# Kernel optimization log

Measured on AMD Instinct MI355X. Metric: run time of the kernel, lower is better.

Reference implementation:

```python
import jax, jax.numpy as jnp
import numpy as np

P = 15          # processor layers
D = 128         # node/edge feature dim (== hidden dim)
N_NODES = 10000
N_EDGES = 160000


def _mlp(x, w0, b0, w1, b1, w2, b2):
    h = jax.nn.relu(x @ w0 + b0)
    h = jax.nn.relu(h @ w1 + b1)
    return h @ w2 + b2


def setup_inputs() -> dict:
    key = jax.random.key(0)
    ks = jax.random.split(key, 20)
    inp = {
        "node_features": jax.random.normal(ks[0], (N_NODES, D), jnp.float32),
        "edge_features": jax.random.normal(ks[1], (N_EDGES, D), jnp.float32),
        "src": jax.random.randint(ks[2], (N_EDGES,), 0, N_NODES, jnp.int32),
        "dst": jax.random.randint(ks[3], (N_EDGES,), 0, N_NODES, jnp.int32),
    }
    s = 0.05
    # edge MLP: input 2*D + D = 384 -> 128 -> 128 -> 128, stacked over P layers
    inp["ew0"] = jax.random.normal(ks[4], (P, 3 * D, D), jnp.float32) * s
    inp["eb0"] = jnp.zeros((P, D), jnp.float32)
    inp["ew1"] = jax.random.normal(ks[5], (P, D, D), jnp.float32) * s
    inp["eb1"] = jnp.zeros((P, D), jnp.float32)
    inp["ew2"] = jax.random.normal(ks[6], (P, D, D), jnp.float32) * s
    inp["eb2"] = jnp.zeros((P, D), jnp.float32)
    # node MLP: input D + D = 256 -> 128 -> 128 -> 128
    inp["nw0"] = jax.random.normal(ks[7], (P, 2 * D, D), jnp.float32) * s
    inp["nb0"] = jnp.zeros((P, D), jnp.float32)
    inp["nw1"] = jax.random.normal(ks[8], (P, D, D), jnp.float32) * s
    inp["nb1"] = jnp.zeros((P, D), jnp.float32)
    inp["nw2"] = jax.random.normal(ks[9], (P, D, D), jnp.float32) * s
    inp["nb2"] = jnp.zeros((P, D), jnp.float32)
    return inp


def reference(node_features, edge_features, src, dst,
              ew0, eb0, ew1, eb1, ew2, eb2,
              nw0, nb0, nw1, nb1, nw2, nb2):
    n, e = node_features, edge_features
    for i in range(P):
        # --- edge block: gather src/dst node feats, edge MLP, residual ---
        cat_e = jnp.concatenate([n[src], n[dst], e], axis=-1)  # [E, 3D]
        e = _mlp(cat_e, ew0[i], eb0[i], ew1[i], eb1[i], ew2[i], eb2[i]) + e
        # --- node block: scatter-sum edges to dst nodes, node MLP, residual ---
        agg = jax.ops.segment_sum(e, dst, num_segments=N_NODES)  # [N, D]
        cat_n = jnp.concatenate([n, agg], axis=-1)               # [N, 2D]
        n = _mlp(cat_n, nw0[i], nb0[i], nw1[i], nb1[i], nw2[i], nb2[i]) + n
    return n
```

## Files before the change

### kernel.cpp

```cpp
#include <hip/hip_runtime.h>

#define DD 128
#define PP 15
#define NNODES 10000
#define NEDGES 160000

typedef __attribute__((ext_vector_type(8))) short bf16x8;
typedef __attribute__((ext_vector_type(4))) float f32x4;

__device__ inline ushort f2bf(float f) {
  unsigned u = __builtin_bit_cast(unsigned, f);
  u += 0x7FFFu + ((u >> 16) & 1u);
  return (ushort)(u >> 16);
}

__device__ inline float bf2f(ushort h) {
  unsigned u = ((unsigned)h) << 16;
  return __builtin_bit_cast(float, u);
}

__device__ inline uint cvt_pk(float lo, float hi) {
  uint r;
  asm("v_cvt_pk_bf16_f32 %0, %1, %2" : "=v"(r) : "v"(lo), "v"(hi));
  return r;
}

__device__ inline f32x4 mfma16(bf16x8 a, bf16x8 b, f32x4 c) {
  return __builtin_amdgcn_mfma_f32_16x16x32_bf16(a, b, c, 0, 0, 0);
}

__global__ __launch_bounds__(256) void pack_all(
    const float* __restrict__ ew0, const float* __restrict__ ew1,
    const float* __restrict__ ew2, const float* __restrict__ nw0,
    const float* __restrict__ nw1, const float* __restrict__ nw2,
    ushort* __restrict__ out) {
  int i = blockIdx.x * 256 + threadIdx.x;
  if (i >= 2211840) return;
  const float* w; int K; int j = i;
  if (i < 737280)       { w = ew0; K = 384; }
  else if (i < 983040)  { w = ew1; K = 128; j = i - 737280; }
  else if (i < 1228800) { w = ew2; K = 128; j = i - 983040; }
  else if (i < 1720320) { w = nw0; K = 256; j = i - 1228800; }
  else if (i < 1966080) { w = nw1; K = 128; j = i - 1720320; }
  else                  { w = nw2; K = 128; j = i - 1966080; }
  int per = K * 128;
  int p = j / per, q = j % per;
  int e = q & 7;
  int lane = (q >> 3) & 63;
  int t = q >> 9;
  int nkt = K >> 5;
  int kt = t % nkt, cb = t / nkt;
  int k = kt * 32 + ((lane >> 4) << 3) + e;
  int n = (cb << 4) + (lane & 15);
  out[i] = f2bf(w[(size_t)p * per + (size_t)k * 128 + n]);
}

__global__ __launch_bounds__(256) void cvt_all(const float* __restrict__ ef,
                                               const float* __restrict__ nf,
                                               ushort* __restrict__ ebf,
                                               float* __restrict__ nbuf,
                                               ushort* __restrict__ nbf) {
  const int en4 = NEDGES * DD / 4;
  const int nn4 = NNODES * DD / 4;
  int i = blockIdx.x * 256 + threadIdx.x;
  if (i < en4) {
    float4 v = ((const float4*)ef)[i];
    ushort4 h;
    h.x = f2bf(v.x); h.y = f2bf(v.y); h.z = f2bf(v.z); h.w = f2bf(v.w);
    ((ushort4*)ebf)[i] = h;
  } else if (i < en4 + nn4) {
    int k = i - en4;
    float4 v = ((const float4*)nf)[k];
    ((float4*)nbuf)[k] = v;
    ushort4 h;
    h.x = f2bf(v.x); h.y = f2bf(v.y); h.z = f2bf(v.z); h.w = f2bf(v.w);
    ((ushort4*)nbf)[k] = h;
  }
}

__global__ __launch_bounds__(256) void hist_kernel(const int* __restrict__ dst,
                                                   int* __restrict__ cnt) {
  int i = blockIdx.x * 256 + threadIdx.x;
  if (i < NEDGES) atomicAdd(&cnt[dst[i]], 1);
}

__global__ __launch_bounds__(256) void scan_kernel(const int* __restrict__ cnt,
                                                   int* __restrict__ row_start,
                                                   int* __restrict__ cursor) {
  __shared__ int part[256];
  const int CH = (NNODES + 255) / 256;
  int t = threadIdx.x;
  int beg = t * CH, end = min(beg + CH, NNODES);
  int s = 0;
  for (int i = beg; i < end; ++i) s += cnt[i];
  part[t] = s;
  __syncthreads();
  for (int off = 1; off < 256; off <<= 1) {
    int v = (t >= off) ? part[t - off] : 0;
    __syncthreads();
    part[t] += v;
    __syncthreads();
  }
  int run = part[t] - s;
  for (int i = beg; i < end; ++i) {
    row_start[i] = run;
    cursor[i] = run;
    run += cnt[i];
  }
  if (t == 255) row_start[NNODES] = NEDGES;
}

__global__ __launch_bounds__(256) void scatter_kernel(const int* __restrict__ dst,
                                                      int* __restrict__ cursor,
                                                      int* __restrict__ eidx) {
  int i = blockIdx.x * 256 + threadIdx.x;
  if (i < NEDGES) {
    int pos = atomicAdd(&cursor[dst[i]], 1);
    eidx[pos] = i;
  }
}

__global__ __launch_bounds__(256) void agg_kernel(const ushort* __restrict__ ebf,
                                                  ushort* __restrict__ abf,
                                                  const int* __restrict__ row_start,
                                                  const int* __restrict__ eidx) {
  int wv = threadIdx.x >> 6, lane = threadIdx.x & 63;
  int node = blockIdx.x * 4 + wv;
  if (node >= NNODES) return;
  int jb = row_start[node], je = row_start[node + 1];
  float ax = 0.f, ay = 0.f, bx = 0.f, by = 0.f;
  float cx = 0.f, cy = 0.f, dx = 0.f, dy = 0.f;
  int j = jb;
  for (; j + 3 < je; j += 4) {
    int e0 = eidx[j], e1 = eidx[j + 1], e2 = eidx[j + 2], e3 = eidx[j + 3];
    uint u0 = *(const uint*)(ebf + (size_t)e0 * DD + lane * 2);
    uint u1 = *(const uint*)(ebf + (size_t)e1 * DD + lane * 2);
    uint u2 = *(const uint*)(ebf + (size_t)e2 * DD + lane * 2);
    uint u3 = *(const uint*)(ebf + (size_t)e3 * DD + lane * 2);
    ax += bf2f((ushort)u0); ay += __builtin_bit_cast(float, u0 & 0xFFFF0000u);
    bx += bf2f((ushort)u1); by += __builtin_bit_cast(float, u1 & 0xFFFF0000u);
    cx += bf2f((ushort)u2); cy += __builtin_bit_cast(float, u2 & 0xFFFF0000u);
    dx += bf2f((ushort)u3); dy += __builtin_bit_cast(float, u3 & 0xFFFF0000u);
  }
  for (; j < je; ++j) {
    int e0 = eidx[j];
    uint u0 = *(const uint*)(ebf + (size_t)e0 * DD + lane * 2);
    ax += bf2f((ushort)u0); ay += __builtin_bit_cast(float, u0 & 0xFFFF0000u);
  }
  float sx = (ax + bx) + (cx + dx);
  float sy = (ay + by) + (cy + dy);
  *(uint*)&abf[(size_t)node * DD + lane * 2] = cvt_pk(sx, sy);
}

__global__ __launch_bounds__(512, 6) void edge_kernel(
    const ushort* __restrict__ nbf, ushort* __restrict__ ebf,
    const int* __restrict__ srcI, const int* __restrict__ dstI,
    const ushort* __restrict__ w0, const float* __restrict__ b0,
    const ushort* __restrict__ w1, const float* __restrict__ b1,
    const ushort* __restrict__ w2, const float* __restrict__ b2) {
  __shared__ ushort S[64 * 384];
  const int tid = threadIdx.x;
  const int e0 = blockIdx.x * 64;
  const int lane = tid & 63, wv = tid >> 6;
  const int l15 = lane & 15, l4 = lane >> 4;

#pragma unroll
  for (int i = 0; i < 6; ++i) {
    int c = i * 512 + tid;
    int row = c / 48, f8 = c % 48;
    const ushort* sp;
    if (f8 < 16)       sp = nbf + (size_t)srcI[e0 + row] * DD + f8 * 8;
    else if (f8 < 32)  sp = nbf + (size_t)dstI[e0 + row] * DD + (f8 - 16) * 8;
    else               sp = ebf + (size_t)(e0 + row) * DD + (f8 - 32) * 8;
    bf16x8 v = *(const bf16x8*)sp;
    *(bf16x8*)&S[row * 384 + ((f8 ^ (row & 15)) * 8)] = v;
  }
  __syncthreads();

  const f32x4 z = {0.f, 0.f, 0.f, 0.f};
  const int cb = wv;
  const int col = cb * 16 + l15;
  f32x4 acc[4];

#pragma unroll
  for (int rb = 0; rb < 4; ++rb) acc[rb] = z;
#pragma unroll
  for (int kt = 0; kt < 12; ++kt) {
    bf16x8 bW = *(const bf16x8*)(w0 + (size_t)((cb * 12 + kt) * 64 + lane) * 8);
#pragma unroll
    for (int rb = 0; rb < 4; ++rb) {
      int row = rb * 16 + l15;
      bf16x8 a = *(const bf16x8*)&S[row * 384 + (((kt * 4 + l4) ^ (row & 15)) * 8)];
      acc[rb] = mfma16(a, bW, acc[rb]);
    }
  }
  __syncthreads();

  {
    float bias = b0[col];
    int cs = col >> 3, c7 = col & 7;
#pragma unroll
    for (int rb = 0; rb < 4; ++rb) {
      float v0 = fmaxf(acc[rb][0] + bias, 0.f);
      float v1 = fmaxf(acc[rb][1] + bias, 0.f);
      float v2 = fmaxf(acc[rb][2] + bias, 0.f);
      float v3 = fmaxf(acc[rb][3] + bias, 0.f);
      uint p01 = cvt_pk(v0, v1), p23 = cvt_pk(v2, v3);
      int r0 = rb * 16 + l4 * 4;
      S[(r0 + 0) * 384 + ((cs ^ ((r0 + 0) & 15)) * 8) + c7] = (ushort)p01;
      S[(r0 + 1) * 384 + ((cs ^ ((r0 + 1) & 15)) * 8) + c7] = (ushort)(p01 >> 16);
      S[(r0 + 2) * 384 + ((cs ^ ((r0 + 2) & 15)) * 8) + c7] = (ushort)p23;
      S[(r0 + 3) * 384 + ((cs ^ ((r0 + 3) & 15)) * 8) + c7] = (ushort)(p23 >> 16);
    }
  }
  __syncthreads();

#pragma unroll
  for (int rb = 0; rb < 4; ++rb) acc[rb] = z;
#pragma unroll
  for (int kt = 0; kt < 4; ++kt) {
    bf16x8 bW = *(const bf16x8*)(w1 + (size_t)((cb * 4 + kt) * 64 + lane) * 8);
#pragma unroll
    for (int rb = 0; rb < 4; ++rb) {
      int row = rb * 16 + l15;
      bf16x8 a = *(const bf16x8*)&S[row * 384 + (((kt * 4 + l4) ^ (row & 15)) * 8)];
      acc[rb] = mfma16(a, bW, acc[rb]);
    }
  }
  {
    float bias = b1[col];
    int cs = col >> 3, c7 = col & 7;
#pragma unroll
    for (int rb = 0; rb < 4; ++rb) {
      float v0 = fmaxf(acc[rb][0] + bias, 0.f);
      float v1 = fmaxf(acc[rb][1] + bias, 0.f);
      float v2 = fmaxf(acc[rb][2] + bias, 0.f);
      float v3 = fmaxf(acc[rb][3] + bias, 0.f);
      uint p01 = cvt_pk(v0, v1), p23 = cvt_pk(v2, v3);
      int r0 = rb * 16 + l4 * 4;
      S[(r0 + 0) * 384 + ((16 + (cs ^ ((r0 + 0) & 15))) * 8) + c7] = (ushort)p01;
      S[(r0 + 1) * 384 + ((16 + (cs ^ ((r0 + 1) & 15))) * 8) + c7] = (ushort)(p01 >> 16);
      S[(r0 + 2) * 384 + ((16 + (cs ^ ((r0 + 2) & 15))) * 8) + c7] = (ushort)p23;
      S[(r0 + 3) * 384 + ((16 + (cs ^ ((r0 + 3) & 15))) * 8) + c7] = (ushort)(p23 >> 16);
    }
  }
  __syncthreads();

#pragma unroll
  for (int rb = 0; rb < 4; ++rb) acc[rb] = z;
#pragma unroll
  for (int kt = 0; kt < 4; ++kt) {
    bf16x8 bW = *(const bf16x8*)(w2 + (size_t)((cb * 4 + kt) * 64 + lane) * 8);
#pragma unroll
    for (int rb = 0; rb < 4; ++rb) {
      int row = rb * 16 + l15;
      bf16x8 a = *(const bf16x8*)&S[row * 384 + ((16 + ((kt * 4 + l4) ^ (row & 15))) * 8)];
      acc[rb] = mfma16(a, bW, acc[rb]);
    }
  }
  {
    float bias = b2[col];
    int cs = col >> 3, c7 = col & 7;
#pragma unroll
    for (int rb = 0; rb < 4; ++rb) {
      int r0 = rb * 16 + l4 * 4;
      int i0 = (r0 + 0) * 384 + ((32 + (cs ^ ((r0 + 0) & 15))) * 8) + c7;
      int i1 = (r0 + 1) * 384 + ((32 + (cs ^ ((r0 + 1) & 15))) * 8) + c7;
      int i2 = (r0 + 2) * 384 + ((32 + (cs ^ ((r0 + 2) & 15))) * 8) + c7;
      int i3 = (r0 + 3) * 384 + ((32 + (cs ^ ((r0 + 3) & 15))) * 8) + c7;
      float v0 = bf2f(S[i0]) + acc[rb][0] + bias;
      float v1 = bf2f(S[i1]) + acc[rb][1] + bias;
      float v2 = bf2f(S[i2]) + acc[rb][2] + bias;
      float v3 = bf2f(S[i3]) + acc[rb][3] + bias;
      uint p01 = cvt_pk(v0, v1), p23 = cvt_pk(v2, v3);
      S[i0] = (ushort)p01;
      S[i1] = (ushort)(p01 >> 16);
      S[i2] = (ushort)p23;
      S[i3] = (ushort)(p23 >> 16);
    }
  }
  __syncthreads();
#pragma unroll
  for (int i = 0; i < 2; ++i) {
    int c = i * 512 + tid;
    int row = c >> 4, f8 = c & 15;
    bf16x8 v = *(const bf16x8*)&S[row * 384 + ((32 + (f8 ^ (row & 15))) * 8)];
    *(bf16x8*)&ebf[(size_t)(e0 + row) * DD + f8 * 8] = v;
  }
}

__global__ __launch_bounds__(256) void node_kernel(
    float* __restrict__ nbuf, ushort* __restrict__ nbf,
    const ushort* __restrict__ abf,
    const ushort* __restrict__ w0, const float* __restrict__ b0,
    const ushort* __restrict__ w1, const float* __restrict__ b1,
    const ushort* __restrict__ w2, const float* __restrict__ b2) {
  __shared__ ushort Alds[32 * 256];
  __shared__ ushort Hlds[32 * 128];
  const int tid = threadIdx.x;
  const int n0 = blockIdx.x * 32;
  const int lane = tid & 63, wv = tid >> 6;
  const int l15 = lane & 15, l4 = lane >> 4;

#pragma unroll
  for (int i = 0; i < 4; ++i) {
    int c = i * 256 + tid;
    int row = c >> 5, f8 = c & 31;
    int node = n0 + row;
    bf16x8 v = {0, 0, 0, 0, 0, 0, 0, 0};
    if (node < NNODES) {
      const ushort* sp = (f8 < 16) ? nbf + (size_t)node * DD + f8 * 8
                                   : abf + (size_t)node * DD + (f8 - 16) * 8;
      v = *(const bf16x8*)sp;
    }
    *(bf16x8*)&Alds[row * 256 + ((f8 ^ (row & 15)) * 8)] = v;
  }
  __syncthreads();

  const f32x4 z = {0.f, 0.f, 0.f, 0.f};
  const int cbA = wv * 2, cbB = wv * 2 + 1;
  f32x4 acc[2][2];

  acc[0][0] = z; acc[0][1] = z; acc[1][0] = z; acc[1][1] = z;
#pragma unroll
  for (int kt = 0; kt < 8; ++kt) {
    bf16x8 bA = *(const bf16x8*)(w0 + (size_t)((cbA * 8 + kt) * 64 + lane) * 8);
    bf16x8 bB = *(const bf16x8*)(w0 + (size_t)((cbB * 8 + kt) * 64 + lane) * 8);
    int sl = ((kt * 4 + l4) ^ l15) * 8;
    bf16x8 a0 = *(const bf16x8*)&Alds[l15 * 256 + sl];
    bf16x8 a1 = *(const bf16x8*)&Alds[(16 + l15) * 256 + sl];
    acc[0][0] = mfma16(a0, bA, acc[0][0]); acc[0][1] = mfma16(a0, bB, acc[0][1]);
    acc[1][0] = mfma16(a1, bA, acc[1][0]); acc[1][1] = mfma16(a1, bB, acc[1][1]);
  }
  {
    float biasA = b0[cbA * 16 + l15], biasB = b0[cbB * 16 + l15];
#pragma unroll
    for (int cbi = 0; cbi < 2; ++cbi) {
      int col = (wv * 2 + cbi) * 16 + l15;
      float bias = cbi ? biasB : biasA;
      int cs = col >> 3, c7 = col & 7;
#pragma unroll
      for (int rb = 0; rb < 2; ++rb) {
        float v0 = fmaxf(acc[rb][cbi][0] + bias, 0.f);
        float v1 = fmaxf(acc[rb][cbi][1] + bias, 0.f);
        float v2 = fmaxf(acc[rb][cbi][2] + bias, 0.f);
        float v3 = fmaxf(acc[rb][cbi][3] + bias, 0.f);
        uint p01 = cvt_pk(v0, v1), p23 = cvt_pk(v2, v3);
        int r0 = rb * 16 + l4 * 4;
        Hlds[(r0 + 0) * 128 + ((cs ^ ((r0 + 0) & 15)) * 8) + c7] = (ushort)p01;
        Hlds[(r0 + 1) * 128 + ((cs ^ ((r0 + 1) & 15)) * 8) + c7] = (ushort)(p01 >> 16);
        Hlds[(r0 + 2) * 128 + ((cs ^ ((r0 + 2) & 15)) * 8) + c7] = (ushort)p23;
        Hlds[(r0 + 3) * 128 + ((cs ^ ((r0 + 3) & 15)) * 8) + c7] = (ushort)(p23 >> 16);
      }
    }
  }
  __syncthreads();

  acc[0][0] = z; acc[0][1] = z; acc[1][0] = z; acc[1][1] = z;
#pragma unroll
  for (int kt = 0; kt < 4; ++kt) {
    bf16x8 bA = *(const bf16x8*)(w1 + (size_t)((cbA * 4 + kt) * 64 + lane) * 8);
    bf16x8 bB = *(const bf16x8*)(w1 + (size_t)((cbB * 4 + kt) * 64 + lane) * 8);
    int sl = ((kt * 4 + l4) ^ l15) * 8;
    bf16x8 a0 = *(const bf16x8*)&Hlds[l15 * 128 + sl];
    bf16x8 a1 = *(const bf16x8*)&Hlds[(16 + l15) * 128 + sl];
    acc[0][0] = mfma16(a0, bA, acc[0][0]); acc[0][1] = mfma16(a0, bB, acc[0][1]);
    acc[1][0] = mfma16(a1, bA, acc[1][0]); acc[1][1] = mfma16(a1, bB, acc[1][1]);
  }
  {
    float biasA = b1[cbA * 16 + l15], biasB = b1[cbB * 16 + l15];
#pragma unroll
    for (int cbi = 0; cbi < 2; ++cbi) {
      int col = (wv * 2 + cbi) * 16 + l15;
      float bias = cbi ? biasB : biasA;
      int cs = col >> 3, c7 = col & 7;
#pragma unroll
      for (int rb = 0; rb < 2; ++rb) {
        float v0 = fmaxf(acc[rb][cbi][0] + bias, 0.f);
        float v1 = fmaxf(acc[rb][cbi][1] + bias, 0.f);
        float v2 = fmaxf(acc[rb][cbi][2] + bias, 0.f);
        float v3 = fmaxf(acc[rb][cbi][3] + bias, 0.f);
        uint p01 = cvt_pk(v0, v1), p23 = cvt_pk(v2, v3);
        int r0 = rb * 16 + l4 * 4;
        Alds[(r0 + 0) * 256 + ((16 + (cs ^ ((r0 + 0) & 15))) * 8) + c7] = (ushort)p01;
        Alds[(r0 + 1) * 256 + ((16 + (cs ^ ((r0 + 1) & 15))) * 8) + c7] = (ushort)(p01 >> 16);
        Alds[(r0 + 2) * 256 + ((16 + (cs ^ ((r0 + 2) & 15))) * 8) + c7] = (ushort)p23;
        Alds[(r0 + 3) * 256 + ((16 + (cs ^ ((r0 + 3) & 15))) * 8) + c7] = (ushort)(p23 >> 16);
      }
    }
  }
  __syncthreads();

  acc[0][0] = z; acc[0][1] = z; acc[1][0] = z; acc[1][1] = z;
#pragma unroll
  for (int kt = 0; kt < 4; ++kt) {
    bf16x8 bA = *(const bf16x8*)(w2 + (size_t)((cbA * 4 + kt) * 64 + lane) * 8);
    bf16x8 bB = *(const bf16x8*)(w2 + (size_t)((cbB * 4 + kt) * 64 + lane) * 8);
    int sl = (16 + ((kt * 4 + l4) ^ l15)) * 8;
    bf16x8 a0 = *(const bf16x8*)&Alds[l15 * 256 + sl];
    bf16x8 a1 = *(const bf16x8*)&Alds[(16 + l15) * 256 + sl];
    acc[0][0] = mfma16(a0, bA, acc[0][0]); acc[0][1] = mfma16(a0, bB, acc[0][1]);
    acc[1][0] = mfma16(a1, bA, acc[1][0]); acc[1][1] = mfma16(a1, bB, acc[1][1]);
  }
  {
#pragma unroll
    for (int cbi = 0; cbi < 2; ++cbi) {
      int col = (wv * 2 + cbi) * 16 + l15;
      float bias = b2[col];
#pragma unroll
      for (int rb = 0; rb < 2; ++rb) {
        int r0 = rb * 16 + l4 * 4;
        float res[4];
#pragma unroll
        for (int r = 0; r < 4; ++r) {
          int node = n0 + r0 + r;
          if (node < NNODES) {
            size_t off = (size_t)node * DD + col;
            res[r] = nbuf[off] + acc[rb][cbi][r] + bias;
            nbuf[off] = res[r];
          } else res[r] = 0.f;
        }
        uint p01 = cvt_pk(res[0], res[1]), p23 = cvt_pk(res[2], res[3]);
#pragma unroll
        for (int r = 0; r < 4; ++r) {
          int node = n0 + r0 + r;
          if (node < NNODES) {
            ushort h = (r == 0) ? (ushort)p01 : (r == 1) ? (ushort)(p01 >> 16)
                     : (r == 2) ? (ushort)p23 : (ushort)(p23 >> 16);
            nbf[(size_t)node * DD + col] = h;
          }
        }
      }
    }
  }
}

extern "C" void kernel_launch(void* const* d_in, const int* in_sizes, int n_in,
                              void* d_out, int out_size, void* d_ws, size_t ws_size,
                              hipStream_t stream) {
  const float* node_f = (const float*)d_in[0];
  const float* edge_f = (const float*)d_in[1];
  const int* srcI = (const int*)d_in[2];
  const int* dstI = (const int*)d_in[3];
  const float* ew0 = (const float*)d_in[4];
  const float* eb0 = (const float*)d_in[5];
  const float* ew1 = (const float*)d_in[6];
  const float* eb1 = (const float*)d_in[7];
  const float* ew2 = (const float*)d_in[8];
  const float* eb2 = (const float*)d_in[9];
  const float* nw0 = (const float*)d_in[10];
  const float* nb0 = (const float*)d_in[11];
  const float* nw1 = (const float*)d_in[12];
  const float* nb1 = (const float*)d_in[13];
  const float* nw2 = (const float*)d_in[14];
  const float* nb2 = (const float*)d_in[15];

  char* ws = (char*)d_ws;
  const size_t NB  = (size_t)NNODES * DD * 4;
  const size_t EBH = (size_t)NEDGES * DD * 2;
  const size_t NBH = (size_t)NNODES * DD * 2;
  ushort* ebf  = (ushort*)ws;
  float*  nbuf = (float*)(ws + EBH);
  ushort* nbf  = (ushort*)(ws + EBH + NB);
  ushort* abf  = (ushort*)(ws + EBH + NB + NBH);
  ushort* pw   = (ushort*)(ws + EBH + NB + 2 * NBH);
  ushort* pew0 = pw;
  ushort* pew1 = pew0 + 737280;
  ushort* pew2 = pew1 + 245760;
  ushort* pnw0 = pew2 + 245760;
  ushort* pnw1 = pnw0 + 491520;
  ushort* pnw2 = pnw1 + 245760;
  const size_t WBYTES = 2211840ull * 2;
  int* eidx      = (int*)(ws + EBH + NB + 2 * NBH + WBYTES);
  int* cnt       = eidx + NEDGES;
  int* row_start = cnt + NNODES;
  int* cursor    = row_start + NNODES + 1;

  pack_all<<<(2211840 + 255) / 256, 256, 0, stream>>>(ew0, ew1, ew2, nw0, nw1,
                                                      nw2, pw);

  hipMemsetAsync(cnt, 0, NNODES * sizeof(int), stream);
  hist_kernel<<<(NEDGES + 255) / 256, 256, 0, stream>>>(dstI, cnt);
  scan_kernel<<<1, 256, 0, stream>>>(cnt, row_start, cursor);
  scatter_kernel<<<(NEDGES + 255) / 256, 256, 0, stream>>>(dstI, cursor, eidx);

  {
    int tot = NEDGES * DD / 4 + NNODES * DD / 4;
    cvt_all<<<(tot + 255) / 256, 256, 0, stream>>>(edge_f, node_f, ebf, nbuf, nbf);
  }

  const int eblocks = NEDGES / 64;
  const int nblocks = (NNODES + 31) / 32;
  const int ablocks = (NNODES + 3) / 4;

  for (int p = 0; p < PP; ++p) {
    edge_kernel<<<eblocks, 512, 0, stream>>>(
        nbf, ebf, srcI, dstI,
        pew0 + (size_t)p * 49152, eb0 + (size_t)p * DD,
        pew1 + (size_t)p * 16384, eb1 + (size_t)p * DD,
        pew2 + (size_t)p * 16384, eb2 + (size_t)p * DD);
    agg_kernel<<<ablocks, 256, 0, stream>>>(ebf, abf, row_start, eidx);
    node_kernel<<<nblocks, 256, 0, stream>>>(
        nbuf, nbf, abf,
        pnw0 + (size_t)p * 32768, nb0 + (size_t)p * DD,
        pnw1 + (size_t)p * 16384, nb1 + (size_t)p * DD,
        pnw2 + (size_t)p * 16384, nb2 + (size_t)p * DD);
  }

  hipMemcpyAsync(d_out, nbuf, NB, hipMemcpyDeviceToDevice, stream);
}
```

Baseline: 1.342 ms.

## Shrink edge kernel LDS by reading edge features directly from global memory

The edge kernel no longer stages the edge-feature third of the concatenated input in shared memory. Its MFMA A operands are loaded straight from global memory, and the residual values are read into registers before the last matmul. This cuts LDS per block from 48KB to 32KB, and the occupancy hint is raised from 6 to 8 to fit more blocks per CU. The cost is uncoalesced 16-byte and 2-byte global reads of edge features, each row read twice, plus higher register pressure under the tighter launch bound.

```diff
diff --git a/kernel.cpp b/kernel.cpp
--- a/kernel.cpp
+++ b/kernel.cpp
@@ -152,28 +152,27 @@
   *(uint*)&abf[(size_t)node * DD + lane * 2] = cvt_pk(sx, sy);
 }
 
-__global__ __launch_bounds__(512, 6) void edge_kernel(
+__global__ __launch_bounds__(512, 8) void edge_kernel(
     const ushort* __restrict__ nbf, ushort* __restrict__ ebf,
     const int* __restrict__ srcI, const int* __restrict__ dstI,
     const ushort* __restrict__ w0, const float* __restrict__ b0,
     const ushort* __restrict__ w1, const float* __restrict__ b1,
     const ushort* __restrict__ w2, const float* __restrict__ b2) {
-  __shared__ ushort S[64 * 384];
+  __shared__ ushort S[64 * 256];
   const int tid = threadIdx.x;
   const int e0 = blockIdx.x * 64;
   const int lane = tid & 63, wv = tid >> 6;
   const int l15 = lane & 15, l4 = lane >> 4;
 
 #pragma unroll
-  for (int i = 0; i < 6; ++i) {
+  for (int i = 0; i < 4; ++i) {
     int c = i * 512 + tid;
-    int row = c / 48, f8 = c % 48;
+    int row = c >> 5, f8 = c & 31;
     const ushort* sp;
-    if (f8 < 16)       sp = nbf + (size_t)srcI[e0 + row] * DD + f8 * 8;
-    else if (f8 < 32)  sp = nbf + (size_t)dstI[e0 + row] * DD + (f8 - 16) * 8;
-    else               sp = ebf + (size_t)(e0 + row) * DD + (f8 - 32) * 8;
+    if (f8 < 16) sp = nbf + (size_t)srcI[e0 + row] * DD + f8 * 8;
+    else         sp = nbf + (size_t)dstI[e0 + row] * DD + (f8 - 16) * 8;
     bf16x8 v = *(const bf16x8*)sp;
-    *(bf16x8*)&S[row * 384 + ((f8 ^ (row & 15)) * 8)] = v;
+    *(bf16x8*)&S[row * 256 + ((f8 ^ (row & 15)) * 8)] = v;
   }
   __syncthreads();
 
@@ -185,13 +184,35 @@
 #pragma unroll
   for (int rb = 0; rb < 4; ++rb) acc[rb] = z;
 #pragma unroll
-  for (int kt = 0; kt < 12; ++kt) {
+  for (int kt = 0; kt < 4; ++kt) {
     bf16x8 bW = *(const bf16x8*)(w0 + (size_t)((cb * 12 + kt) * 64 + lane) * 8);
 #pragma unroll
     for (int rb = 0; rb < 4; ++rb) {
       int row = rb * 16 + l15;
-      bf16x8 a = *(const bf16x8*)&S[row * 384 + (((kt * 4 + l4) ^ (row & 15)) * 8)];
+      bf16x8 a = *(const bf16x8*)&S[row * 256 + (((kt * 4 + l4) ^ (row & 15)) * 8)];
       acc[rb] = mfma16(a, bW, acc[rb]);
+    }
+  }
+#pragma unroll
+  for (int kt = 0; kt < 4; ++kt) {
+    bf16x8 bW = *(const bf16x8*)(w0 + (size_t)((cb * 12 + 4 + kt) * 64 + lane) * 8);
+#pragma unroll
+    for (int rb = 0; rb < 4; ++rb) {
+      int row = rb * 16 + l15;
+      bf16x8 a = *(const bf16x8*)&S[row * 256 + ((16 + ((kt * 4 + l4) ^ (row & 15))) * 8)];
+      acc[rb] = mfma16(a, bW, acc[rb]);
+    }
+  }
+  {
+    const ushort* ep = ebf + (size_t)(e0 + l15) * DD + l4 * 8;
+#pragma unroll
+    for (int kt = 0; kt < 4; ++kt) {
+      bf16x8 bW = *(const bf16x8*)(w0 + (size_t)((cb * 12 + 8 + kt) * 64 + lane) * 8);
+#pragma unroll
+      for (int rb = 0; rb < 4; ++rb) {
+        bf16x8 a = *(const bf16x8*)(ep + rb * 16 * DD + kt * 32);
+        acc[rb] = mfma16(a, bW, acc[rb]);
+      }
     }
   }
   __syncthreads();
@@ -207,10 +228,10 @@
       float v3 = fmaxf(acc[rb][3] + bias, 0.f);
       uint p01 = cvt_pk(v0, v1), p23 = cvt_pk(v2, v3);
       int r0 = rb * 16 + l4 * 4;
-      S[(r0 + 0) * 384 + ((cs ^ ((r0 + 0) & 15)) * 8) + c7] = (ushort)p01;
-      S[(r0 + 1) * 384 + ((cs ^ ((r0 + 1) & 15)) * 8) + c7] = (ushort)(p01 >> 16);
-      S[(r0 + 2) * 384 + ((cs ^ ((r0 + 2) & 15)) * 8) + c7] = (ushort)p23;
-      S[(r0 + 3) * 384 + ((cs ^ ((r0 + 3) & 15)) * 8) + c7] = (ushort)(p23 >> 16);
+      S[(r0 + 0) * 256 + ((cs ^ ((r0 + 0) & 15)) * 8) + c7] = (ushort)p01;
+      S[(r0 + 1) * 256 + ((cs ^ ((r0 + 1) & 15)) * 8) + c7] = (ushort)(p01 >> 16);
+      S[(r0 + 2) * 256 + ((cs ^ ((r0 + 2) & 15)) * 8) + c7] = (ushort)p23;
+      S[(r0 + 3) * 256 + ((cs ^ ((r0 + 3) & 15)) * 8) + c7] = (ushort)(p23 >> 16);
     }
   }
   __syncthreads();
@@ -223,7 +244,7 @@
 #pragma unroll
     for (int rb = 0; rb < 4; ++rb) {
       int row = rb * 16 + l15;
-      bf16x8 a = *(const bf16x8*)&S[row * 384 + (((kt * 4 + l4) ^ (row & 15)) * 8)];
+      bf16x8 a = *(const bf16x8*)&S[row * 256 + (((kt * 4 + l4) ^ (row & 15)) * 8)];
       acc[rb] = mfma16(a, bW, acc[rb]);
     }
   }
@@ -238,14 +259,20 @@
       float v3 = fmaxf(acc[rb][3] + bias, 0.f);
       uint p01 = cvt_pk(v0, v1), p23 = cvt_pk(v2, v3);
       int r0 = rb * 16 + l4 * 4;
-      S[(r0 + 0) * 384 + ((16 + (cs ^ ((r0 + 0) & 15))) * 8) + c7] = (ushort)p01;
-      S[(r0 + 1) * 384 + ((16 + (cs ^ ((r0 + 1) & 15))) * 8) + c7] = (ushort)(p01 >> 16);
-      S[(r0 + 2) * 384 + ((16 + (cs ^ ((r0 + 2) & 15))) * 8) + c7] = (ushort)p23;
-      S[(r0 + 3) * 384 + ((16 + (cs ^ ((r0 + 3) & 15))) * 8) + c7] = (ushort)(p23 >> 16);
-    }
-  }
-  __syncthreads();
-
+      S[(r0 + 0) * 256 + ((16 + (cs ^ ((r0 + 0) & 15))) * 8) + c7] = (ushort)p01;
+      S[(r0 + 1) * 256 + ((16 + (cs ^ ((r0 + 1) & 15))) * 8) + c7] = (ushort)(p01 >> 16);
+      S[(r0 + 2) * 256 + ((16 + (cs ^ ((r0 + 2) & 15))) * 8) + c7] = (ushort)p23;
+      S[(r0 + 3) * 256 + ((16 + (cs ^ ((r0 + 3) & 15))) * 8) + c7] = (ushort)(p23 >> 16);
+    }
+  }
+  __syncthreads();
+
+  ushort er[4][4];
+#pragma unroll
+  for (int rb = 0; rb < 4; ++rb)
+#pragma unroll
+    for (int r = 0; r < 4; ++r)
+      er[rb][r] = ebf[(size_t)(e0 + rb * 16 + l4 * 4 + r) * DD + col];
 #pragma unroll
   for (int rb = 0; rb < 4; ++rb) acc[rb] = z;
 #pragma unroll
@@ -254,7 +281,7 @@
 #pragma unroll
     for (int rb = 0; rb < 4; ++rb) {
       int row = rb * 16 + l15;
-      bf16x8 a = *(const bf16x8*)&S[row * 384 + ((16 + ((kt * 4 + l4) ^ (row & 15))) * 8)];
+      bf16x8 a = *(const bf16x8*)&S[row * 256 + ((16 + ((kt * 4 + l4) ^ (row & 15))) * 8)];
       acc[rb] = mfma16(a, bW, acc[rb]);
     }
   }
@@ -263,20 +290,16 @@
     int cs = col >> 3, c7 = col & 7;
 #pragma unroll
     for (int rb = 0; rb < 4; ++rb) {
+      float v0 = bf2f(er[rb][0]) + acc[rb][0] + bias;
+      float v1 = bf2f(er[rb][1]) + acc[rb][1] + bias;
+      float v2 = bf2f(er[rb][2]) + acc[rb][2] + bias;
+      float v3 = bf2f(er[rb][3]) + acc[rb][3] + bias;
+      uint p01 = cvt_pk(v0, v1), p23 = cvt_pk(v2, v3);
       int r0 = rb * 16 + l4 * 4;
-      int i0 = (r0 + 0) * 384 + ((32 + (cs ^ ((r0 + 0) & 15))) * 8) + c7;
-      int i1 = (r0 + 1) * 384 + ((32 + (cs ^ ((r0 + 1) & 15))) * 8) + c7;
-      int i2 = (r0 + 2) * 384 + ((32 + (cs ^ ((r0 + 2) & 15))) * 8) + c7;
-      int i3 = (r0 + 3) * 384 + ((32 + (cs ^ ((r0 + 3) & 15))) * 8) + c7;
-      float v0 = bf2f(S[i0]) + acc[rb][0] + bias;
-      float v1 = bf2f(S[i1]) + acc[rb][1] + bias;
-      float v2 = bf2f(S[i2]) + acc[rb][2] + bias;
-      float v3 = bf2f(S[i3]) + acc[rb][3] + bias;
-      uint p01 = cvt_pk(v0, v1), p23 = cvt_pk(v2, v3);
-      S[i0] = (ushort)p01;
-      S[i1] = (ushort)(p01 >> 16);
-      S[i2] = (ushort)p23;
-      S[i3] = (ushort)(p23 >> 16);
+      S[(r0 + 0) * 256 + ((cs ^ ((r0 + 0) & 15)) * 8) + c7] = (ushort)p01;
+      S[(r0 + 1) * 256 + ((cs ^ ((r0 + 1) & 15)) * 8) + c7] = (ushort)(p01 >> 16);
+      S[(r0 + 2) * 256 + ((cs ^ ((r0 + 2) & 15)) * 8) + c7] = (ushort)p23;
+      S[(r0 + 3) * 256 + ((cs ^ ((r0 + 3) & 15)) * 8) + c7] = (ushort)(p23 >> 16);
     }
   }
   __syncthreads();
@@ -284,7 +307,7 @@
   for (int i = 0; i < 2; ++i) {
     int c = i * 512 + tid;
     int row = c >> 4, f8 = c & 15;
-    bf16x8 v = *(const bf16x8*)&S[row * 384 + ((32 + (f8 ^ (row & 15))) * 8)];
+    bf16x8 v = *(const bf16x8*)&S[row * 256 + ((f8 ^ (row & 15)) * 8)];
     *(bf16x8*)&ebf[(size_t)(e0 + row) * DD + f8 * 8] = v;
   }
 }
```

After: 1.530 ms. 1.14x slower.
